# Kernel tuning notes

Measured on AMD Instinct MI355X. Metric: run time of the kernel, lower is better.

Reference implementation:

```python
import jax, jax.numpy as jnp
import numpy as np

N_HEADS = 16


def setup_inputs() -> dict:
    key = jax.random.key(0)
    ks = jax.random.split(key, 5)
    B, S, D = 2, 2048, 1024
    x = jax.random.normal(ks[0], (B, S, D), dtype=jnp.float32)
    Wqkv = jax.random.normal(ks[1], (D, 3 * D), dtype=jnp.float32) * (1.0 / np.sqrt(D))
    bqkv = jax.random.normal(ks[2], (3 * D,), dtype=jnp.float32) * 0.02
    Wout = jax.random.normal(ks[3], (D, D), dtype=jnp.float32) * (1.0 / np.sqrt(D))
    bout = jax.random.normal(ks[4], (D,), dtype=jnp.float32) * 0.02
    return {"x": x, "Wqkv": Wqkv, "bqkv": bqkv, "Wout": Wout, "bout": bout}


def reference(x, Wqkv, bqkv, Wout, bout):
    B, S, D = x.shape
    H = N_HEADS
    dh = D // H
    # qkv projection, then view as [B,S,H,3*dh] and chunk on last dim
    # (matches torch: per-head q/k/v are interleaved slices of the projection)
    qkv = (x @ Wqkv + bqkv).reshape(B, S, H, 3 * dh).transpose(0, 2, 1, 3)  # [B,H,S,3dh]
    q, k, v = jnp.split(qkv, 3, axis=-1)  # each [B,H,S,dh]
    scale = jnp.asarray(1.0 / np.sqrt(dh), dtype=x.dtype)
    scores = jnp.einsum('bhqd,bhkd->bhqk', q, k) * scale  # [B,H,S,S]
    causal = jnp.tril(jnp.ones((S, S), dtype=bool))
    scores = jnp.where(causal, scores, jnp.asarray(-jnp.inf, dtype=scores.dtype))
    attn_w = jax.nn.softmax(scores, axis=-1)
    attn = jnp.einsum('bhqk,bhkd->bhqd', attn_w, v)  # [B,H,S,dh]
    attn = attn.transpose(0, 2, 1, 3).reshape(B, S, D)
    return attn @ Wout + bout
```

## Files before the change

### kernel.cpp

```cpp
#include <hip/hip_runtime.h>
#include <hip/hip_bf16.h>
#include <cstdint>
#include <cstddef>

typedef __hip_bfloat16 bf16;
typedef short bf16x4 __attribute__((ext_vector_type(4)));
typedef short bf16x8 __attribute__((ext_vector_type(8)));
typedef float f32x4 __attribute__((ext_vector_type(4)));

#define LOG2E 1.44269504088896f

static constexpr int Bb = 2, S = 2048, D = 1024, H = 16, DH = 64;

struct TrueT  { static constexpr bool value = true;  };
struct FalseT { static constexpr bool value = false; };

__device__ inline short f2bf_bits(float f) {
  bf16 b = __float2bfloat16(f);
  short s;
  __builtin_memcpy(&s, &b, 2);
  return s;
}
__device__ inline float bfbits2f(short s) {
  uint32_t u = ((uint32_t)(uint16_t)s) << 16;
  float f;
  __builtin_memcpy(&f, &u, 4);
  return f;
}

__global__ __launch_bounds__(256) void prep_kernel(
    const float* __restrict__ Wqkv, bf16* __restrict__ wqkvT,
    const float* __restrict__ Wout, bf16* __restrict__ woutT,
    const float* __restrict__ x, bf16* __restrict__ xbf) {
  const int blk = blockIdx.x;
  const int tid = threadIdx.x;
  if (blk < 4096) {
    __shared__ float t[32][33];
    const float* in;
    bf16* out;
    int R, C, bx, by;
    if (blk < 3072) { in = Wqkv; out = wqkvT; R = 1024; C = 3072; bx = blk % 96; by = blk / 96; }
    else            { in = Wout; out = woutT; R = 1024; C = 1024; bx = (blk - 3072) % 32; by = (blk - 3072) / 32; }
    int c0 = bx * 32, r0 = by * 32;
    int tx = tid & 31, ty = tid >> 5;
#pragma unroll
    for (int i = 0; i < 4; i++) {
      int r = ty + i * 8;
      t[r][tx] = in[(size_t)(r0 + r) * C + c0 + tx];
    }
    __syncthreads();
#pragma unroll
    for (int i = 0; i < 4; i++) {
      int c = ty + i * 8;
      out[(size_t)(c0 + c) * R + r0 + tx] = __float2bfloat16(t[tx][c]);
    }
  } else {
    size_t i = ((size_t)(blk - 4096) * 256 + tid) * 8;
    f32x4 a = *(const f32x4*)(x + i);
    f32x4 b = *(const f32x4*)(x + i + 4);
    bf16x8 v;
#pragma unroll
    for (int j = 0; j < 4; j++) { v[j] = f2bf_bits(a[j]); v[4 + j] = f2bf_bits(b[j]); }
    *(bf16x8*)((short*)xbf + i) = v;
  }
}

__global__ __launch_bounds__(256) void gemm_qkv(
    const bf16* __restrict__ A, const bf16* __restrict__ Bt,
    const float* __restrict__ bias,
    bf16* __restrict__ Qb, bf16* __restrict__ Kb, bf16* __restrict__ Vtb) {
  constexpr int K = 1024;
  __shared__ __align__(16) short smA[128 * 32];
  __shared__ __align__(16) short smB[128 * 32];
  __shared__ __align__(16) short smE[4][16 * 72];

  const int tid = threadIdx.x;
  const int wave = tid >> 6, lane = tid & 63;
  const int quad = lane >> 4, l16 = lane & 15;
  const int m0 = blockIdx.y * 128, n0 = blockIdx.x * 128;
  const int wm = wave >> 1, wn = wave & 1;

  f32x4 acc[4][4];
#pragma unroll
  for (int i = 0; i < 4; i++)
#pragma unroll
    for (int j = 0; j < 4; j++) acc[i][j] = {0.f, 0.f, 0.f, 0.f};

  const int srow = lane >> 2;
  const int scol = (lane & 3) * 8;

  for (int k0 = 0; k0 < K; k0 += 32) {
#pragma unroll
    for (int half = 0; half < 2; half++) {
      int row = half * 64 + wave * 16 + srow;
      const bf16* ga = A + (size_t)(m0 + row) * K + k0 + scol;
      const bf16* gb = Bt + (size_t)(n0 + row) * K + k0 + scol;
      __builtin_amdgcn_global_load_lds(
          (const __attribute__((address_space(1))) void*)ga,
          (__attribute__((address_space(3))) void*)&smA[(half * 64 + wave * 16) * 32],
          16, 0, 0);
      __builtin_amdgcn_global_load_lds(
          (const __attribute__((address_space(1))) void*)gb,
          (__attribute__((address_space(3))) void*)&smB[(half * 64 + wave * 16) * 32],
          16, 0, 0);
    }
    __syncthreads();

    bf16x8 af[4], bf_[4];
#pragma unroll
    for (int mi = 0; mi < 4; mi++)
      af[mi] = *(const bf16x8*)&smA[(wm * 64 + mi * 16 + l16) * 32 + quad * 8];
#pragma unroll
    for (int ni = 0; ni < 4; ni++)
      bf_[ni] = *(const bf16x8*)&smB[(wn * 64 + ni * 16 + l16) * 32 + quad * 8];
#pragma unroll
    for (int mi = 0; mi < 4; mi++)
#pragma unroll
      for (int ni = 0; ni < 4; ni++)
        acc[mi][ni] = __builtin_amdgcn_mfma_f32_16x16x32_bf16(
            af[mi], bf_[ni], acc[mi][ni], 0, 0, 0);
    __syncthreads();
  }

  const int cs0 = n0 + wn * 64;
  const int h = cs0 / 192;
  const int rt = (cs0 >> 6) % 3;
  const int t0w = m0 + wm * 64;
  const int b = t0w >> 11, s0w = t0w & 2047;

  float bv[4];
#pragma unroll
  for (int ni = 0; ni < 4; ni++) bv[ni] = bias[cs0 + ni * 16 + l16];

  if (rt < 2) {
    const float qscale = (rt == 0) ? (0.125f * LOG2E) : 1.0f;
    bf16* dst = (rt == 0 ? Qb : Kb) + ((size_t)(b * H + h) * S + s0w) * 64;
    short* sE = &smE[wave][0];
    const int r8 = lane >> 2, s4 = lane & 3;
#pragma unroll
    for (int mi = 0; mi < 4; mi++) {
#pragma unroll
      for (int ni = 0; ni < 4; ni++)
#pragma unroll
        for (int r = 0; r < 4; r++)
          sE[(quad * 4 + r) * 72 + ni * 16 + l16] =
              f2bf_bits((acc[mi][ni][r] + bv[ni]) * qscale);
      asm volatile("s_waitcnt lgkmcnt(0)" ::: "memory");
      bf16x8 w0 = *(const bf16x8*)&sE[r8 * 72 + s4 * 16];
      bf16x8 w1 = *(const bf16x8*)&sE[r8 * 72 + s4 * 16 + 8];
      short* g = (short*)dst + (size_t)(mi * 16 + r8) * 64 + s4 * 16;
      *(bf16x8*)g = w0;
      *(bf16x8*)(g + 8) = w1;
      asm volatile("s_waitcnt lgkmcnt(0)" ::: "memory");
    }
  } else {
#pragma unroll
    for (int ni = 0; ni < 4; ni++) {
      const int dh = ni * 16 + l16;
#pragma unroll
      for (int mi = 0; mi < 4; mi++) {
        const int s0 = s0w + mi * 16 + quad * 4;
        size_t base = ((size_t)(b * H + h) * 64 + dh) * S + s0;
        bf16x4 vv;
#pragma unroll
        for (int r = 0; r < 4; r++) vv[r] = f2bf_bits(acc[mi][ni][r] + bv[ni]);
        *(bf16x4*)((short*)Vtb + base) = vv;
      }
    }
  }
}

__global__ __launch_bounds__(256) void gemm_out(
    const bf16* __restrict__ A, const bf16* __restrict__ Bt,
    const float* __restrict__ bias, float* __restrict__ C,
    int M, int N, int K) {
  constexpr int BN = 64, NF = 2;
  __shared__ __align__(16) short smA[128 * 32];
  __shared__ __align__(16) short smB[BN * 32];
  __shared__ __align__(16) float smEf[4][580];

  const int tid = threadIdx.x;
  const int wave = tid >> 6, lane = tid & 63;
  const int quad = lane >> 4, l16 = lane & 15;
  const int m0 = blockIdx.y * 128, n0 = blockIdx.x * BN;
  const int wm = wave >> 1, wn = wave & 1;

  f32x4 acc[4][NF];
#pragma unroll
  for (int i = 0; i < 4; i++)
#pragma unroll
    for (int j = 0; j < NF; j++) acc[i][j] = {0.f, 0.f, 0.f, 0.f};

  const int srow = lane >> 2;
  const int scol = (lane & 3) * 8;

  for (int k0 = 0; k0 < K; k0 += 32) {
#pragma unroll
    for (int half = 0; half < 2; half++) {
      int row = half * 64 + wave * 16 + srow;
      const bf16* ga = A + (size_t)(m0 + row) * K + k0 + scol;
      __builtin_amdgcn_global_load_lds(
          (const __attribute__((address_space(1))) void*)ga,
          (__attribute__((address_space(3))) void*)&smA[(half * 64 + wave * 16) * 32],
          16, 0, 0);
    }
    {
      int row = wave * 16 + srow;
      const bf16* gb = Bt + (size_t)(n0 + row) * K + k0 + scol;
      __builtin_amdgcn_global_load_lds(
          (const __attribute__((address_space(1))) void*)gb,
          (__attribute__((address_space(3))) void*)&smB[(wave * 16) * 32],
          16, 0, 0);
    }
    __syncthreads();

    bf16x8 af[4], bf_[NF];
#pragma unroll
    for (int mi = 0; mi < 4; mi++)
      af[mi] = *(const bf16x8*)&smA[(wm * 64 + mi * 16 + l16) * 32 + quad * 8];
#pragma unroll
    for (int ni = 0; ni < NF; ni++)
      bf_[ni] = *(const bf16x8*)&smB[(wn * 32 + ni * 16 + l16) * 32 + quad * 8];
#pragma unroll
    for (int mi = 0; mi < 4; mi++)
#pragma unroll
      for (int ni = 0; ni < NF; ni++)
        acc[mi][ni] = __builtin_amdgcn_mfma_f32_16x16x32_bf16(
            af[mi], bf_[ni], acc[mi][ni], 0, 0, 0);
    __syncthreads();
  }

  float bv[NF];
#pragma unroll
  for (int ni = 0; ni < NF; ni++) bv[ni] = bias[n0 + wn * 32 + ni * 16 + l16];

  float* sE = &smEf[wave][0];
#pragma unroll
  for (int mi = 0; mi < 4; mi++) {
#pragma unroll
    for (int ni = 0; ni < NF; ni++)
#pragma unroll
      for (int r = 0; r < 4; r++)
        sE[(quad * 4 + r) * 36 + ni * 16 + l16] = acc[mi][ni][r] + bv[ni];
    asm volatile("s_waitcnt lgkmcnt(0)" ::: "memory");
#pragma unroll
    for (int t = 0; t < 2; t++) {
      int slot = t * 64 + lane;
      int rr = slot >> 3, c4 = slot & 7;
      f32x4 v = *(const f32x4*)&sE[rr * 36 + c4 * 4];
      int row = m0 + wm * 64 + mi * 16 + rr;
      int col = n0 + wn * 32 + c4 * 4;
      *(f32x4*)&C[(size_t)row * N + col] = v;
    }
    asm volatile("s_waitcnt lgkmcnt(0)" ::: "memory");
  }
}

__global__ __launch_bounds__(256) void attn_kernel(
    const bf16* __restrict__ Qb, const bf16* __restrict__ Kb,
    const bf16* __restrict__ Vtb,
    bf16* __restrict__ Op0, bf16* __restrict__ Op1, bf16* __restrict__ Op2,
    float* __restrict__ lp0, float* __restrict__ lp1, float* __restrict__ lp2,
    bf16* __restrict__ Ofinal, int split) {
  const int blk = blockIdx.x;
  const int xcd = blk & 7;
  const int idx = blk >> 3;
  int sk, p, bh;
  if (split == 3)      { bh = xcd + 8 * (idx / 48); int r = idx % 48; p = r & 15; sk = r >> 4; }
  else if (split == 2) { bh = xcd + 8 * (idx / 32); int r = idx % 32; p = r & 15; sk = r >> 4; }
  else                 { bh = xcd + 8 * (idx / 16); p = idx & 15; sk = 0; }
  const int h = bh & (H - 1), b = bh >> 4;
  const int tid = threadIdx.x;
  const int wave = tid >> 6, lane = tid & 63;
  const int quad = lane >> 4, l16 = lane & 15;

  bf16*  __restrict__ Op = (sk == 0) ? Op0 : (sk == 1) ? Op1 : Op2;
  float* __restrict__ lp = (sk == 0) ? lp0 : (sk == 1) ? lp1 : lp2;

  const bf16* Qh = Qb + (size_t)(b * H + h) * S * 64;
  const bf16* Kh = Kb + (size_t)(b * H + h) * S * 64;
  const bf16* Vth = Vtb + (size_t)(b * H + h) * 64 * S;

  __shared__ __align__(16) short smK[2][64 * 64];
  __shared__ __align__(16) short smVt[2][64 * 64];
  __shared__ __align__(16) short pLds[4][16][76];

  const int lrow = lane >> 3;
  const int lg = lane & 7;
  const int swz = l16 & 7;

  bf16x8 onesB;
#pragma unroll
  for (int j = 0; j < 8; j++) onesB[j] = (short)0x3F80;

  auto stage = [&](int it2, int bufi) {
    const int kv0 = it2 * 64;
#pragma unroll
    for (int j = 0; j < 2; j++) {
      const int row = wave * 16 + j * 8 + lrow;
      const bf16* ks = Kh + (size_t)(kv0 + row) * 64 + (lg ^ (row & 7)) * 8;
      __builtin_amdgcn_global_load_lds(
          (const __attribute__((address_space(1))) void*)ks,
          (__attribute__((address_space(3))) void*)&smK[bufi][(wave * 16 + j * 8) * 64],
          16, 0, 0);
      const bf16* vs = Vth + (size_t)row * S + kv0 + (lg ^ (row & 7)) * 8;
      __builtin_amdgcn_global_load_lds(
          (const __attribute__((address_space(1))) void*)vs,
          (__attribute__((address_space(3))) void*)&smVt[bufi][(wave * 16 + j * 8) * 64],
          16, 0, 0);
    }
  };

#pragma unroll
  for (int pass = 0; pass < 2; pass++) {
    const int qt = pass ? p : (31 - p);
    const int q0 = qt * 64 + wave * 16;
    const int qglob = q0 + l16;

    bf16x8 aQ[2];
#pragma unroll
    for (int kh = 0; kh < 2; kh++)
      aQ[kh] = *(const bf16x8*)(Qh + (size_t)(q0 + l16) * 64 + kh * 32 + quad * 8);

    f32x4 o[4];
#pragma unroll
    for (int dt = 0; dt < 4; dt++) o[dt] = {0.f, 0.f, 0.f, 0.f};
    f32x4 lacc = {0.f, 0.f, 0.f, 0.f};

    auto compute_tile = [&](int it2, int bufi, auto diag_tag) {
      constexpr bool DIAG = decltype(diag_tag)::value;
      const int kv0 = it2 * 64;

      f32x4 z[4];
#pragma unroll
      for (int nh = 0; nh < 4; nh++) {
        const int row = nh * 16 + l16;
        f32x4 t = {0.f, 0.f, 0.f, 0.f};
#pragma unroll
        for (int kh = 0; kh < 2; kh++) {
          bf16x8 bK = *(const bf16x8*)&smK[bufi][row * 64 + ((kh * 4 + quad) ^ swz) * 8];
          t = __builtin_amdgcn_mfma_f32_16x16x32_bf16(bK, aQ[kh], t, 0, 0, 0);
        }
        z[nh] = t;
      }

#pragma unroll
      for (int nh = 0; nh < 4; nh++) {
        bf16x4 pk;
#pragma unroll
        for (int r = 0; r < 4; r++) {
          float e = exp2f(z[nh][r]);
          if (DIAG) {
            const int kidx = kv0 + nh * 16 + quad * 4 + r;
            e = (kidx <= qglob) ? e : 0.f;
          }
          pk[r] = f2bf_bits(e);
        }
        *(bf16x4*)&pLds[wave][l16][nh * 16 + quad * 4] = pk;
      }

      asm volatile("s_waitcnt lgkmcnt(0)" ::: "memory");

      bf16x8 aP[2];
#pragma unroll
      for (int k2 = 0; k2 < 2; k2++)
        aP[k2] = *(const bf16x8*)&pLds[wave][l16][k2 * 32 + quad * 8];
#pragma unroll
      for (int k2 = 0; k2 < 2; k2++)
        lacc = __builtin_amdgcn_mfma_f32_16x16x32_bf16(aP[k2], onesB, lacc, 0, 0, 0);
#pragma unroll
      for (int dt = 0; dt < 4; dt++) {
        const int row = dt * 16 + l16;
#pragma unroll
        for (int k2 = 0; k2 < 2; k2++) {
          bf16x8 bV = *(const bf16x8*)&smVt[bufi][row * 64 + ((k2 * 4 + quad) ^ swz) * 8];
          o[dt] = __builtin_amdgcn_mfma_f32_16x16x32_bf16(aP[k2], bV, o[dt], 0, 0, 0);
        }
      }
    };

    int it = sk;
    __syncthreads();
    if (it <= qt) stage(it, 0);
    __syncthreads();
    int cur = 0;
    while (it <= qt) {
      const int next = it + split;
      if (next <= qt) stage(next, cur ^ 1);
      if (it == qt) compute_tile(it, cur, TrueT{});
      else          compute_tile(it, cur, FalseT{});
      __syncthreads();
      cur ^= 1;
      it = next;
    }

    if (split > 1) {
      const size_t rowbase = (size_t)(b * H + h) * S + q0;
      if (l16 == 0) {
#pragma unroll
        for (int r = 0; r < 4; r++) lp[rowbase + quad * 4 + r] = lacc[r];
      }
#pragma unroll
      for (int r = 0; r < 4; r++) {
        const size_t row = rowbase + quad * 4 + r;
#pragma unroll
        for (int dt = 0; dt < 4; dt++)
          ((short*)Op)[row * 64 + dt * 16 + l16] = f2bf_bits(o[dt][r]);
      }
    } else {
#pragma unroll
      for (int r = 0; r < 4; r++) {
        const float inv = 1.f / lacc[r];
        const int q = q0 + quad * 4 + r;
#pragma unroll
        for (int dt = 0; dt < 4; dt++)
          Ofinal[(size_t)(b * S + q) * D + h * 64 + dt * 16 + l16] =
              __float2bfloat16(o[dt][r] * inv);
      }
    }
  }
}

__global__ __launch_bounds__(256) void attn_reduce(
    const bf16* __restrict__ O0, const bf16* __restrict__ O1,
    const bf16* __restrict__ O2,
    const float* __restrict__ l0, const float* __restrict__ l1,
    const float* __restrict__ l2,
    bf16* __restrict__ attnO, int nparts) {
  int gid = blockIdx.x * 256 + threadIdx.x;
  int row = gid >> 3;
  int c8 = (gid & 7) * 8;
  float lsum = l0[row] + l1[row];
  if (nparts == 3) lsum += l2[row];
  float inv = 1.f / lsum;
  bf16x8 a = *(const bf16x8*)((const short*)O0 + (size_t)row * 64 + c8);
  bf16x8 bb = *(const bf16x8*)((const short*)O1 + (size_t)row * 64 + c8);
  float acc[8];
#pragma unroll
  for (int j = 0; j < 8; j++) acc[j] = bfbits2f(a[j]) + bfbits2f(bb[j]);
  if (nparts == 3) {
    bf16x8 c = *(const bf16x8*)((const short*)O2 + (size_t)row * 64 + c8);
#pragma unroll
    for (int j = 0; j < 8; j++) acc[j] += bfbits2f(c[j]);
  }
  bf16x8 o;
#pragma unroll
  for (int j = 0; j < 8; j++) o[j] = f2bf_bits(acc[j] * inv);
  int bh = row >> 11, q = row & 2047;
  int b = bh >> 4, h = bh & 15;
  *(bf16x8*)((short*)attnO + (((size_t)(b * S + q) * H + h) * 64 + c8)) = o;
}

extern "C" void kernel_launch(void* const* d_in, const int* in_sizes, int n_in,
                              void* d_out, int out_size, void* d_ws, size_t ws_size,
                              hipStream_t stream) {
  const float* x    = (const float*)d_in[0];
  const float* Wqkv = (const float*)d_in[1];
  const float* bqkv = (const float*)d_in[2];
  const float* Wout = (const float*)d_in[3];
  const float* bout = (const float*)d_in[4];
  float* out = (float*)d_out;

  char* ws = (char*)d_ws;
  int split;
  if (ws_size >= 59506688)      split = 3;
  else if (ws_size >= 50855936) split = 2;
  else                          split = 1;

  bf16* Qb  = (bf16*)(ws);
  bf16* Kb  = (bf16*)(ws + 8388608);
  bf16* Vtb = (bf16*)(ws + 16777216);
  bf16* xbf = (bf16*)(ws + 25165824);

  bf16 *Op0 = nullptr, *Op1 = nullptr, *Op2 = nullptr, *attnO;
  float *lp0 = nullptr, *lp1 = nullptr, *lp2 = nullptr;
  bf16 *wqkvT, *woutT;
  if (split == 3) {
    Op0   = (bf16*)(ws + 25165824);
    Op1   = (bf16*)(ws + 33554432);
    Op2   = (bf16*)(ws + 41943040);
    lp0   = (float*)(ws + 50331648);
    lp1   = (float*)(ws + 50593792);
    lp2   = (float*)(ws + 50855936);
    attnO = (bf16*)(ws + 8388608);
    wqkvT = (bf16*)(ws + 51118080);
    woutT = (bf16*)(ws + 57409536);
  } else if (split == 2) {
    Op0   = (bf16*)(ws + 25165824);
    Op1   = (bf16*)(ws + 33554432);
    lp0   = (float*)(ws + 41943040);
    lp1   = (float*)(ws + 42205184);
    attnO = (bf16*)(ws + 8388608);
    wqkvT = (bf16*)(ws + 42467328);
    woutT = (bf16*)(ws + 48758784);
  } else {
    attnO = (bf16*)(ws + 25165824);
    wqkvT = (bf16*)(ws + 33554432);
    woutT = (bf16*)(ws + 39845888);
  }

  prep_kernel<<<dim3(6144), 256, 0, stream>>>(Wqkv, wqkvT, Wout, woutT, x, xbf);

  gemm_qkv<<<dim3(3072 / 128, 4096 / 128), 256, 0, stream>>>(
      xbf, wqkvT, bqkv, Qb, Kb, Vtb);

  if (split == 3) {
    attn_kernel<<<dim3(1536), 256, 0, stream>>>(
        Qb, Kb, Vtb, Op0, Op1, Op2, lp0, lp1, lp2, nullptr, 3);
    attn_reduce<<<dim3(2048), 256, 0, stream>>>(Op0, Op1, Op2, lp0, lp1, lp2, attnO, 3);
  } else if (split == 2) {
    attn_kernel<<<dim3(1024), 256, 0, stream>>>(
        Qb, Kb, Vtb, Op0, Op1, Op0, lp0, lp1, lp0, nullptr, 2);
    attn_reduce<<<dim3(2048), 256, 0, stream>>>(Op0, Op1, Op0, lp0, lp1, lp0, attnO, 2);
  } else {
    attn_kernel<<<dim3(512), 256, 0, stream>>>(
        Qb, Kb, Vtb, nullptr, nullptr, nullptr, nullptr, nullptr, nullptr, attnO, 1);
  }

  gemm_out<<<dim3(1024 / 64, 4096 / 128), 256, 0, stream>>>(
      attnO, woutT, bout, out, 4096, 1024, 1024);
}
```

Baseline: 189.4 us.

## Coalesce attention output stores via LDS, swizzle P buffer, drop three-way split

Attention output tiles are now staged through the per-wave P scratch in LDS so that each lane writes full 16-byte vectors to global memory instead of scattered 2-byte stores. The padded P scratch is replaced by an XOR-swizzled layout to cut LDS footprint while avoiding bank conflicts. Wave priority is raised around the MFMA sections. The three-way KV split path is removed, so large workspaces now use the two-way split, which changes parallelism and reduce cost.

```diff
diff --git a/kernel.cpp b/kernel.cpp
--- a/kernel.cpp
+++ b/kernel.cpp
@@ -259,23 +259,22 @@
 __global__ __launch_bounds__(256) void attn_kernel(
     const bf16* __restrict__ Qb, const bf16* __restrict__ Kb,
     const bf16* __restrict__ Vtb,
-    bf16* __restrict__ Op0, bf16* __restrict__ Op1, bf16* __restrict__ Op2,
-    float* __restrict__ lp0, float* __restrict__ lp1, float* __restrict__ lp2,
+    bf16* __restrict__ Op0, bf16* __restrict__ Op1,
+    float* __restrict__ lp0, float* __restrict__ lp1,
     bf16* __restrict__ Ofinal, int split) {
   const int blk = blockIdx.x;
   const int xcd = blk & 7;
   const int idx = blk >> 3;
   int sk, p, bh;
-  if (split == 3)      { bh = xcd + 8 * (idx / 48); int r = idx % 48; p = r & 15; sk = r >> 4; }
-  else if (split == 2) { bh = xcd + 8 * (idx / 32); int r = idx % 32; p = r & 15; sk = r >> 4; }
-  else                 { bh = xcd + 8 * (idx / 16); p = idx & 15; sk = 0; }
+  if (split == 2) { bh = xcd + 8 * (idx / 32); int r = idx % 32; p = r & 15; sk = r >> 4; }
+  else            { bh = xcd + 8 * (idx / 16); p = idx & 15; sk = 0; }
   const int h = bh & (H - 1), b = bh >> 4;
   const int tid = threadIdx.x;
   const int wave = tid >> 6, lane = tid & 63;
   const int quad = lane >> 4, l16 = lane & 15;
 
-  bf16*  __restrict__ Op = (sk == 0) ? Op0 : (sk == 1) ? Op1 : Op2;
-  float* __restrict__ lp = (sk == 0) ? lp0 : (sk == 1) ? lp1 : lp2;
+  bf16*  __restrict__ Op = sk ? Op1 : Op0;
+  float* __restrict__ lp = sk ? lp1 : lp0;
 
   const bf16* Qh = Qb + (size_t)(b * H + h) * S * 64;
   const bf16* Kh = Kb + (size_t)(b * H + h) * S * 64;
@@ -283,11 +282,12 @@
 
   __shared__ __align__(16) short smK[2][64 * 64];
   __shared__ __align__(16) short smVt[2][64 * 64];
-  __shared__ __align__(16) short pLds[4][16][76];
+  __shared__ __align__(16) short pLds[4][16][64];
 
   const int lrow = lane >> 3;
   const int lg = lane & 7;
   const int swz = l16 & 7;
+  const int psw = (l16 & 7) << 1;
 
   bf16x8 onesB;
 #pragma unroll
@@ -332,6 +332,7 @@
       const int kv0 = it2 * 64;
 
       f32x4 z[4];
+      __builtin_amdgcn_s_setprio(1);
 #pragma unroll
       for (int nh = 0; nh < 4; nh++) {
         const int row = nh * 16 + l16;
@@ -343,6 +344,7 @@
         }
         z[nh] = t;
       }
+      __builtin_amdgcn_s_setprio(0);
 
 #pragma unroll
       for (int nh = 0; nh < 4; nh++) {
@@ -356,15 +358,19 @@
           }
           pk[r] = f2bf_bits(e);
         }
-        *(bf16x4*)&pLds[wave][l16][nh * 16 + quad * 4] = pk;
+        const int gw = (nh * 4 + quad) ^ psw;
+        *(bf16x4*)&pLds[wave][l16][gw * 4] = pk;
       }
 
       asm volatile("s_waitcnt lgkmcnt(0)" ::: "memory");
 
       bf16x8 aP[2];
 #pragma unroll
-      for (int k2 = 0; k2 < 2; k2++)
-        aP[k2] = *(const bf16x8*)&pLds[wave][l16][k2 * 32 + quad * 8];
+      for (int k2 = 0; k2 < 2; k2++) {
+        const int gr = (k2 * 8 + quad * 2) ^ psw;
+        aP[k2] = *(const bf16x8*)&pLds[wave][l16][gr * 4];
+      }
+      __builtin_amdgcn_s_setprio(1);
 #pragma unroll
       for (int k2 = 0; k2 < 2; k2++)
         lacc = __builtin_amdgcn_mfma_f32_16x16x32_bf16(aP[k2], onesB, lacc, 0, 0, 0);
@@ -377,6 +383,7 @@
           o[dt] = __builtin_amdgcn_mfma_f32_16x16x32_bf16(aP[k2], bV, o[dt], 0, 0, 0);
         }
       }
+      __builtin_amdgcn_s_setprio(0);
     };
 
     int it = sk;
@@ -394,6 +401,8 @@
       it = next;
     }
 
+    const int rl = lane >> 2, cq = lane & 3;
+    short* pw = &pLds[wave][0][0];
     if (split > 1) {
       const size_t rowbase = (size_t)(b * H + h) * S + q0;
       if (l16 == 0) {
@@ -401,51 +410,51 @@
         for (int r = 0; r < 4; r++) lp[rowbase + quad * 4 + r] = lacc[r];
       }
 #pragma unroll
-      for (int r = 0; r < 4; r++) {
-        const size_t row = rowbase + quad * 4 + r;
-#pragma unroll
-        for (int dt = 0; dt < 4; dt++)
-          ((short*)Op)[row * 64 + dt * 16 + l16] = f2bf_bits(o[dt][r]);
-      }
+      for (int dt = 0; dt < 4; dt++)
+#pragma unroll
+        for (int r = 0; r < 4; r++)
+          pw[(quad * 4 + r) * 64 + dt * 16 + l16] = f2bf_bits(o[dt][r]);
+      asm volatile("s_waitcnt lgkmcnt(0)" ::: "memory");
+      bf16x8 w0 = *(const bf16x8*)&pw[rl * 64 + cq * 16];
+      bf16x8 w1 = *(const bf16x8*)&pw[rl * 64 + cq * 16 + 8];
+      short* g = (short*)Op + (rowbase + rl) * 64 + cq * 16;
+      *(bf16x8*)g = w0;
+      *(bf16x8*)(g + 8) = w1;
+      asm volatile("s_waitcnt lgkmcnt(0)" ::: "memory");
     } else {
-#pragma unroll
-      for (int r = 0; r < 4; r++) {
-        const float inv = 1.f / lacc[r];
-        const int q = q0 + quad * 4 + r;
-#pragma unroll
-        for (int dt = 0; dt < 4; dt++)
-          Ofinal[(size_t)(b * S + q) * D + h * 64 + dt * 16 + l16] =
-              __float2bfloat16(o[dt][r] * inv);
-      }
+      float invr[4];
+#pragma unroll
+      for (int r = 0; r < 4; r++) invr[r] = 1.f / lacc[r];
+#pragma unroll
+      for (int dt = 0; dt < 4; dt++)
+#pragma unroll
+        for (int r = 0; r < 4; r++)
+          pw[(quad * 4 + r) * 64 + dt * 16 + l16] = f2bf_bits(o[dt][r] * invr[r]);
+      asm volatile("s_waitcnt lgkmcnt(0)" ::: "memory");
+      bf16x8 w0 = *(const bf16x8*)&pw[rl * 64 + cq * 16];
+      bf16x8 w1 = *(const bf16x8*)&pw[rl * 64 + cq * 16 + 8];
+      short* g = (short*)Ofinal + (size_t)(b * S + q0 + rl) * D + h * 64 + cq * 16;
+      *(bf16x8*)g = w0;
+      *(bf16x8*)(g + 8) = w1;
+      asm volatile("s_waitcnt lgkmcnt(0)" ::: "memory");
     }
   }
 }
 
 __global__ __launch_bounds__(256) void attn_reduce(
     const bf16* __restrict__ O0, const bf16* __restrict__ O1,
-    const bf16* __restrict__ O2,
     const float* __restrict__ l0, const float* __restrict__ l1,
-    const float* __restrict__ l2,
-    bf16* __restrict__ attnO, int nparts) {
+    bf16* __restrict__ attnO) {
   int gid = blockIdx.x * 256 + threadIdx.x;
   int row = gid >> 3;
   int c8 = (gid & 7) * 8;
-  float lsum = l0[row] + l1[row];
-  if (nparts == 3) lsum += l2[row];
-  float inv = 1.f / lsum;
+  float inv = 1.f / (l0[row] + l1[row]);
   bf16x8 a = *(const bf16x8*)((const short*)O0 + (size_t)row * 64 + c8);
   bf16x8 bb = *(const bf16x8*)((const short*)O1 + (size_t)row * 64 + c8);
-  float acc[8];
-#pragma unroll
-  for (int j = 0; j < 8; j++) acc[j] = bfbits2f(a[j]) + bfbits2f(bb[j]);
-  if (nparts == 3) {
-    bf16x8 c = *(const bf16x8*)((const short*)O2 + (size_t)row * 64 + c8);
-#pragma unroll
-    for (int j = 0; j < 8; j++) acc[j] += bfbits2f(c[j]);
-  }
   bf16x8 o;
 #pragma unroll
-  for (int j = 0; j < 8; j++) o[j] = f2bf_bits(acc[j] * inv);
+  for (int j = 0; j < 8; j++)
+    o[j] = f2bf_bits((bfbits2f(a[j]) + bfbits2f(bb[j])) * inv);
   int bh = row >> 11, q = row & 2047;
   int b = bh >> 4, h = bh & 15;
   *(bf16x8*)((short*)attnO + (((size_t)(b * S + q) * H + h) * 64 + c8)) = o;
@@ -462,30 +471,17 @@
   float* out = (float*)d_out;
 
   char* ws = (char*)d_ws;
-  int split;
-  if (ws_size >= 59506688)      split = 3;
-  else if (ws_size >= 50855936) split = 2;
-  else                          split = 1;
+  const bool split2 = (ws_size >= 50855936);
 
   bf16* Qb  = (bf16*)(ws);
   bf16* Kb  = (bf16*)(ws + 8388608);
   bf16* Vtb = (bf16*)(ws + 16777216);
   bf16* xbf = (bf16*)(ws + 25165824);
 
-  bf16 *Op0 = nullptr, *Op1 = nullptr, *Op2 = nullptr, *attnO;
-  float *lp0 = nullptr, *lp1 = nullptr, *lp2 = nullptr;
+  bf16 *Op0 = nullptr, *Op1 = nullptr, *attnO;
+  float *lp0 = nullptr, *lp1 = nullptr;
   bf16 *wqkvT, *woutT;
-  if (split == 3) {
-    Op0   = (bf16*)(ws + 25165824);
-    Op1   = (bf16*)(ws + 33554432);
-    Op2   = (bf16*)(ws + 41943040);
-    lp0   = (float*)(ws + 50331648);
-    lp1   = (float*)(ws + 50593792);
-    lp2   = (float*)(ws + 50855936);
-    attnO = (bf16*)(ws + 8388608);
-    wqkvT = (bf16*)(ws + 51118080);
-    woutT = (bf16*)(ws + 57409536);
-  } else if (split == 2) {
+  if (split2) {
     Op0   = (bf16*)(ws + 25165824);
     Op1   = (bf16*)(ws + 33554432);
     lp0   = (float*)(ws + 41943040);
@@ -504,17 +500,13 @@
   gemm_qkv<<<dim3(3072 / 128, 4096 / 128), 256, 0, stream>>>(
       xbf, wqkvT, bqkv, Qb, Kb, Vtb);
 
-  if (split == 3) {
-    attn_kernel<<<dim3(1536), 256, 0, stream>>>(
-        Qb, Kb, Vtb, Op0, Op1, Op2, lp0, lp1, lp2, nullptr, 3);
-    attn_reduce<<<dim3(2048), 256, 0, stream>>>(Op0, Op1, Op2, lp0, lp1, lp2, attnO, 3);
-  } else if (split == 2) {
+  if (split2) {
     attn_kernel<<<dim3(1024), 256, 0, stream>>>(
-        Qb, Kb, Vtb, Op0, Op1, Op0, lp0, lp1, lp0, nullptr, 2);
-    attn_reduce<<<dim3(2048), 256, 0, stream>>>(Op0, Op1, Op0, lp0, lp1, lp0, attnO, 2);
+        Qb, Kb, Vtb, Op0, Op1, lp0, lp1, nullptr, 2);
+    attn_reduce<<<dim3(2048), 256, 0, stream>>>(Op0, Op1, lp0, lp1, attnO);
   } else {
     attn_kernel<<<dim3(512), 256, 0, stream>>>(
-        Qb, Kb, Vtb, nullptr, nullptr, nullptr, nullptr, nullptr, nullptr, attnO, 1);
+        Qb, Kb, Vtb, nullptr, nullptr, nullptr, nullptr, attnO, 1);
   }
 
   gemm_out<<<dim3(1024 / 64, 4096 / 128), 256, 0, stream>>>(
```

Result: slower. 194.7 us (+2.8%).

## Process 128-row query tiles per block to reuse staged K/V tiles

Applied to the files above, without the earlier changes.

Each attention block now handles two 64-row query halves (128 rows) against every staged K/V tile, so each K/V load from global memory into LDS feeds twice the MFMA work. The grid is halved and the split-K index mapping is changed so it interleaves splits within each query-tile pair. The cost is more registers (two sets of Q fragments and output accumulators) and fewer blocks. That can lower occupancy and leave the 256 CUs with less work to balance.

```diff
diff --git a/kernel.cpp b/kernel.cpp
--- a/kernel.cpp
+++ b/kernel.cpp
@@ -266,9 +266,9 @@
   const int xcd = blk & 7;
   const int idx = blk >> 3;
   int sk, p, bh;
-  if (split == 3)      { bh = xcd + 8 * (idx / 48); int r = idx % 48; p = r & 15; sk = r >> 4; }
-  else if (split == 2) { bh = xcd + 8 * (idx / 32); int r = idx % 32; p = r & 15; sk = r >> 4; }
-  else                 { bh = xcd + 8 * (idx / 16); p = idx & 15; sk = 0; }
+  if (split == 3)      { bh = xcd + 8 * (idx / 24); int r = idx % 24; p = r / 3; sk = r % 3; }
+  else if (split == 2) { bh = xcd + 8 * (idx / 16); int r = idx % 16; p = r >> 1; sk = r & 1; }
+  else                 { bh = xcd + 8 * (idx >> 3); p = idx & 7; sk = 0; }
   const int h = bh & (H - 1), b = bh >> 4;
   const int tid = threadIdx.x;
   const int wave = tid >> 6, lane = tid & 63;
@@ -313,24 +313,27 @@
 
 #pragma unroll
   for (int pass = 0; pass < 2; pass++) {
-    const int qt = pass ? p : (31 - p);
-    const int q0 = qt * 64 + wave * 16;
-    const int qglob = q0 + l16;
-
-    bf16x8 aQ[2];
-#pragma unroll
-    for (int kh = 0; kh < 2; kh++)
-      aQ[kh] = *(const bf16x8*)(Qh + (size_t)(q0 + l16) * 64 + kh * 32 + quad * 8);
-
-    f32x4 o[4];
-#pragma unroll
-    for (int dt = 0; dt < 4; dt++) o[dt] = {0.f, 0.f, 0.f, 0.f};
-    f32x4 lacc = {0.f, 0.f, 0.f, 0.f};
-
-    auto compute_tile = [&](int it2, int bufi, auto diag_tag) {
+    const int qt = pass ? p : (15 - p);
+    const int q0 = qt * 128 + wave * 16;
+    const int qg0 = q0 + l16;
+    const int qg1 = q0 + 64 + l16;
+    const int itmax = 2 * qt + 1;
+
+    bf16x8 aQ0[2], aQ1[2];
+#pragma unroll
+    for (int kh = 0; kh < 2; kh++) {
+      aQ0[kh] = *(const bf16x8*)(Qh + (size_t)(q0 + l16) * 64 + kh * 32 + quad * 8);
+      aQ1[kh] = *(const bf16x8*)(Qh + (size_t)(q0 + 64 + l16) * 64 + kh * 32 + quad * 8);
+    }
+
+    f32x4 o0[4], o1[4];
+#pragma unroll
+    for (int dt = 0; dt < 4; dt++) { o0[dt] = {0.f, 0.f, 0.f, 0.f}; o1[dt] = {0.f, 0.f, 0.f, 0.f}; }
+    f32x4 lacc0 = {0.f, 0.f, 0.f, 0.f}, lacc1 = {0.f, 0.f, 0.f, 0.f};
+
+    auto compute_half = [&](const bf16x8* aQh, f32x4* oh, f32x4& lacch,
+                            int qglobh, int kv0, int bufi, auto diag_tag) {
       constexpr bool DIAG = decltype(diag_tag)::value;
-      const int kv0 = it2 * 64;
-
       f32x4 z[4];
 #pragma unroll
       for (int nh = 0; nh < 4; nh++) {
@@ -339,7 +342,7 @@
 #pragma unroll
         for (int kh = 0; kh < 2; kh++) {
           bf16x8 bK = *(const bf16x8*)&smK[bufi][row * 64 + ((kh * 4 + quad) ^ swz) * 8];
-          t = __builtin_amdgcn_mfma_f32_16x16x32_bf16(bK, aQ[kh], t, 0, 0, 0);
+          t = __builtin_amdgcn_mfma_f32_16x16x32_bf16(bK, aQh[kh], t, 0, 0, 0);
         }
         z[nh] = t;
       }
@@ -352,7 +355,7 @@
           float e = exp2f(z[nh][r]);
           if (DIAG) {
             const int kidx = kv0 + nh * 16 + quad * 4 + r;
-            e = (kidx <= qglob) ? e : 0.f;
+            e = (kidx <= qglobh) ? e : 0.f;
           }
           pk[r] = f2bf_bits(e);
         }
@@ -367,55 +370,71 @@
         aP[k2] = *(const bf16x8*)&pLds[wave][l16][k2 * 32 + quad * 8];
 #pragma unroll
       for (int k2 = 0; k2 < 2; k2++)
-        lacc = __builtin_amdgcn_mfma_f32_16x16x32_bf16(aP[k2], onesB, lacc, 0, 0, 0);
+        lacch = __builtin_amdgcn_mfma_f32_16x16x32_bf16(aP[k2], onesB, lacch, 0, 0, 0);
 #pragma unroll
       for (int dt = 0; dt < 4; dt++) {
         const int row = dt * 16 + l16;
 #pragma unroll
         for (int k2 = 0; k2 < 2; k2++) {
           bf16x8 bV = *(const bf16x8*)&smVt[bufi][row * 64 + ((k2 * 4 + quad) ^ swz) * 8];
-          o[dt] = __builtin_amdgcn_mfma_f32_16x16x32_bf16(aP[k2], bV, o[dt], 0, 0, 0);
+          oh[dt] = __builtin_amdgcn_mfma_f32_16x16x32_bf16(aP[k2], bV, oh[dt], 0, 0, 0);
         }
       }
+      asm volatile("s_waitcnt lgkmcnt(0)" ::: "memory");
     };
 
     int it = sk;
     __syncthreads();
-    if (it <= qt) stage(it, 0);
+    if (it <= itmax) stage(it, 0);
     __syncthreads();
     int cur = 0;
-    while (it <= qt) {
+    while (it <= itmax) {
       const int next = it + split;
-      if (next <= qt) stage(next, cur ^ 1);
-      if (it == qt) compute_tile(it, cur, TrueT{});
-      else          compute_tile(it, cur, FalseT{});
+      if (next <= itmax) stage(next, cur ^ 1);
+      const int kv0 = it * 64;
+      if (it <= 2 * qt) {
+        if (it == 2 * qt) compute_half(aQ0, o0, lacc0, qg0, kv0, cur, TrueT{});
+        else              compute_half(aQ0, o0, lacc0, qg0, kv0, cur, FalseT{});
+      }
+      if (it == itmax) compute_half(aQ1, o1, lacc1, qg1, kv0, cur, TrueT{});
+      else             compute_half(aQ1, o1, lacc1, qg1, kv0, cur, FalseT{});
       __syncthreads();
       cur ^= 1;
       it = next;
     }
 
     if (split > 1) {
-      const size_t rowbase = (size_t)(b * H + h) * S + q0;
-      if (l16 == 0) {
-#pragma unroll
-        for (int r = 0; r < 4; r++) lp[rowbase + quad * 4 + r] = lacc[r];
-      }
-#pragma unroll
-      for (int r = 0; r < 4; r++) {
-        const size_t row = rowbase + quad * 4 + r;
-#pragma unroll
-        for (int dt = 0; dt < 4; dt++)
-          ((short*)Op)[row * 64 + dt * 16 + l16] = f2bf_bits(o[dt][r]);
+#pragma unroll
+      for (int half = 0; half < 2; half++) {
+        const f32x4* oh = half ? o1 : o0;
+        const f32x4& lh = half ? lacc1 : lacc0;
+        const size_t rowbase = (size_t)(b * H + h) * S + q0 + half * 64;
+        if (l16 == 0) {
+#pragma unroll
+          for (int r = 0; r < 4; r++) lp[rowbase + quad * 4 + r] = lh[r];
+        }
+#pragma unroll
+        for (int r = 0; r < 4; r++) {
+          const size_t row = rowbase + quad * 4 + r;
+#pragma unroll
+          for (int dt = 0; dt < 4; dt++)
+            ((short*)Op)[row * 64 + dt * 16 + l16] = f2bf_bits(oh[dt][r]);
+        }
       }
     } else {
 #pragma unroll
-      for (int r = 0; r < 4; r++) {
-        const float inv = 1.f / lacc[r];
-        const int q = q0 + quad * 4 + r;
-#pragma unroll
-        for (int dt = 0; dt < 4; dt++)
-          Ofinal[(size_t)(b * S + q) * D + h * 64 + dt * 16 + l16] =
-              __float2bfloat16(o[dt][r] * inv);
+      for (int half = 0; half < 2; half++) {
+        const f32x4* oh = half ? o1 : o0;
+        const f32x4& lh = half ? lacc1 : lacc0;
+#pragma unroll
+        for (int r = 0; r < 4; r++) {
+          const float inv = 1.f / lh[r];
+          const int q = q0 + half * 64 + quad * 4 + r;
+#pragma unroll
+          for (int dt = 0; dt < 4; dt++)
+            Ofinal[(size_t)(b * S + q) * D + h * 64 + dt * 16 + l16] =
+                __float2bfloat16(oh[dt][r] * inv);
+        }
       }
     }
   }
@@ -505,15 +524,15 @@
       xbf, wqkvT, bqkv, Qb, Kb, Vtb);
 
   if (split == 3) {
-    attn_kernel<<<dim3(1536), 256, 0, stream>>>(
+    attn_kernel<<<dim3(768), 256, 0, stream>>>(
         Qb, Kb, Vtb, Op0, Op1, Op2, lp0, lp1, lp2, nullptr, 3);
     attn_reduce<<<dim3(2048), 256, 0, stream>>>(Op0, Op1, Op2, lp0, lp1, lp2, attnO, 3);
   } else if (split == 2) {
-    attn_kernel<<<dim3(1024), 256, 0, stream>>>(
+    attn_kernel<<<dim3(512), 256, 0, stream>>>(
         Qb, Kb, Vtb, Op0, Op1, Op0, lp0, lp1, lp0, nullptr, 2);
     attn_reduce<<<dim3(2048), 256, 0, stream>>>(Op0, Op1, Op0, lp0, lp1, lp0, attnO, 2);
   } else {
-    attn_kernel<<<dim3(512), 256, 0, stream>>>(
+    attn_kernel<<<dim3(256), 256, 0, stream>>>(
         Qb, Kb, Vtb, nullptr, nullptr, nullptr, nullptr, nullptr, nullptr, attnO, 1);
   }
 
```

Measured after the change: 203.5 us. 1.07x slower.
